# Kernel tuning notes

Measured on AMD Instinct MI355X. Metric: run time of the kernel, lower is better.

The kernel has to match this reference:

```python
import jax, jax.numpy as jnp
import numpy as np

B, D, H, T = 8192, 256, 266, 20  # batch, dim, dim+10, num timesteps
LAMBDA = 1.0
SIGMA = 1.0
EPS = 1e-5  # torch BatchNorm1d default eps


def _bn(h, g, b):
    # training-mode BatchNorm1d: biased batch statistics over axis 0
    m = h.mean(0)
    v = h.var(0)
    return g * (h - m) * jax.lax.rsqrt(v + EPS) + b


def _hidden(x, W, b, g, be):
    return jax.nn.relu(_bn(x @ W.T + b, g, be))


def setup_inputs() -> dict:
    key = jax.random.key(0)
    ks = jax.random.split(key, 16)

    def n(k, shape, s=0.05):
        return jax.random.normal(k, shape, jnp.float32) * s

    inp = {}
    inp["x"] = jax.random.normal(ks[0], (B, D), jnp.float32)
    inp["xi"] = jax.random.normal(ks[1], (T, B, D), jnp.float32)
    inp["timegrid"] = jnp.linspace(0.0, 1.0, T + 1).astype(jnp.float32)
    # per-timestep stacks of Linear+BN params (i_h1, h1_h2, h2_o)
    inp["W1"] = n(ks[2], (T, H, D)); inp["b1"] = jnp.zeros((T, H), jnp.float32)
    inp["g1"] = jnp.ones((T, H), jnp.float32); inp["be1"] = jnp.zeros((T, H), jnp.float32)
    inp["W2"] = n(ks[3], (T, H, H)); inp["b2"] = jnp.zeros((T, H), jnp.float32)
    inp["g2"] = jnp.ones((T, H), jnp.float32); inp["be2"] = jnp.zeros((T, H), jnp.float32)
    inp["W3"] = n(ks[4], (T, D, H)); inp["b3"] = jnp.zeros((T, D), jnp.float32)
    # v0 network: hiddenLayer(D,H) -> hiddenLayer(H,H) -> hiddenLayer(H,1)
    inp["vW1"] = n(ks[5], (H, D)); inp["vb1"] = jnp.zeros((H,), jnp.float32)
    inp["vg1"] = jnp.ones((H,), jnp.float32); inp["vbe1"] = jnp.zeros((H,), jnp.float32)
    inp["vW2"] = n(ks[6], (H, H)); inp["vb2"] = jnp.zeros((H,), jnp.float32)
    inp["vg2"] = jnp.ones((H,), jnp.float32); inp["vbe2"] = jnp.zeros((H,), jnp.float32)
    inp["vW3"] = n(ks[7], (1, H)); inp["vb3"] = jnp.zeros((1,), jnp.float32)
    inp["vg3"] = jnp.ones((1,), jnp.float32); inp["vbe3"] = jnp.zeros((1,), jnp.float32)
    return inp


def reference(x, xi, timegrid, W1, b1, g1, be1, W2, b2, g2, be2, W3, b3,
              vW1, vb1, vg1, vbe1, vW2, vb2, vg2, vbe2, vW3, vb3, vg3, vbe3):
    # v0 sub-network evaluated on the initial x (i == 0 branch)
    v0 = _hidden(x, vW1, vb1, vg1, vbe1)
    v0 = _hidden(v0, vW2, vb2, vg2, vbe2)
    v0 = _hidden(v0, vW3, vb3, vg3, vbe3)  # [B, 1]

    hsteps = timegrid[1:] - timegrid[:-1]  # [T]

    def step(carry, inp_t):
        xt, vt = carry
        (W1t, b1t, g1t, be1t, W2t, b2t, g2t, be2t, W3t, b3t, ht, xit) = inp_t
        h1 = _hidden(xt, W1t, b1t, g1t, be1t)
        h2 = _hidden(h1, W2t, b2t, g2t, be2t)
        grad = h2 @ W3t.T + b3t                     # [B, D]
        alpha = -jnp.sqrt(LAMBDA) * grad
        f = jnp.sum(alpha * alpha, axis=1)          # ||alpha||_2^2 per row
        noise = SIGMA * jnp.sqrt(ht) * xit          # sigma*sqrt(h)*xi
        # diag(grad @ noise.T) == row-wise dot product (same math, O(B*D))
        dot = jnp.sum(grad * noise, axis=1)
        vt = vt - (f * ht)[:, None] + dot[:, None]
        xt = xt + alpha * ht + noise
        return (xt, vt), None

    (xT, vT), _ = jax.lax.scan(
        step, (x, v0),
        (W1, b1, g1, be1, W2, b2, g2, be2, W3, b3, hsteps, xi))
    return vT, xT
```

## Files before the change

kernel.cpp:

```cpp
#include <hip/hip_runtime.h>
#include <hip/hip_bf16.h>
#include <math.h>

#define BATCH 8192
#define DDIM 256
#define HDIM 266
#define NPAD 320
#define TSTEPS 20
#define BN_EPS 1e-5f
#define LSTR 72

typedef __attribute__((ext_vector_type(8))) short short8;
typedef __attribute__((ext_vector_type(4))) float f32x4;

__device__ __forceinline__ short f2bf(float f) {
    __hip_bfloat16 h = __float2bfloat16(f);
    return *reinterpret_cast<short*>(&h);
}
__device__ __forceinline__ float bf2f(short s) {
    union { unsigned u; float f; } v;
    v.u = ((unsigned)(unsigned short)s) << 16;
    return v.f;
}

#define SZ_W1B (20L * 320 * 256)
#define SZ_W2B (20L * 320 * 320)
#define SZ_W3B (20L * 256 * 320)
#define SZ_VW1 (320L * 256)
#define SZ_VW2 (320L * 320)
#define SZ_B1P (20L * 320)
#define SZ_B2P (20L * 320)
#define PREP_TOTAL (SZ_W1B + SZ_W2B + SZ_W3B + SZ_VW1 + SZ_VW2 + SZ_B1P + SZ_B2P + 3 * 320)

__global__ __launch_bounds__(256)
void prep_k(short* __restrict__ W1b, const float* __restrict__ W1,
            short* __restrict__ W2b, const float* __restrict__ W2,
            short* __restrict__ W3b, const float* __restrict__ W3,
            short* __restrict__ vW1b, const float* __restrict__ vW1,
            short* __restrict__ vW2b, const float* __restrict__ vW2,
            float* __restrict__ b1p, const float* __restrict__ b1,
            float* __restrict__ b2p, const float* __restrict__ b2,
            float* __restrict__ vb1p, const float* __restrict__ vb1,
            float* __restrict__ vb2p, const float* __restrict__ vb2,
            float* __restrict__ vW3p, const float* __restrict__ vW3)
{
    long idx = (long)blockIdx.x * 256 + threadIdx.x;
    if (idx < SZ_W1B) {
        long k = idx % 256, r = (idx / 256) % 320, t = idx / (256L * 320);
        float v = (r < HDIM) ? W1[((size_t)t * HDIM + r) * 256 + k] : 0.0f;
        W1b[idx] = f2bf(v); return;
    }
    idx -= SZ_W1B;
    if (idx < SZ_W2B) {
        long k = idx % 320, r = (idx / 320) % 320, t = idx / (320L * 320);
        float v = (r < HDIM && k < HDIM) ? W2[((size_t)t * HDIM + r) * HDIM + k] : 0.0f;
        W2b[idx] = f2bf(v); return;
    }
    idx -= SZ_W2B;
    if (idx < SZ_W3B) {
        long k = idx % 320, r = (idx / 320) % 256, t = idx / (320L * 256);
        float v = (k < HDIM) ? W3[((size_t)t * 256 + r) * HDIM + k] : 0.0f;
        W3b[idx] = f2bf(v); return;
    }
    idx -= SZ_W3B;
    if (idx < SZ_VW1) {
        long k = idx % 256, r = idx / 256;
        float v = (r < HDIM) ? vW1[(size_t)r * 256 + k] : 0.0f;
        vW1b[idx] = f2bf(v); return;
    }
    idx -= SZ_VW1;
    if (idx < SZ_VW2) {
        long k = idx % 320, r = idx / 320;
        float v = (r < HDIM && k < HDIM) ? vW2[(size_t)r * HDIM + k] : 0.0f;
        vW2b[idx] = f2bf(v); return;
    }
    idx -= SZ_VW2;
    if (idx < SZ_B1P) { long n = idx % 320, t = idx / 320;
        b1p[idx] = (n < HDIM) ? b1[(size_t)t * HDIM + n] : 0.0f; return; }
    idx -= SZ_B1P;
    if (idx < SZ_B2P) { long n = idx % 320, t = idx / 320;
        b2p[idx] = (n < HDIM) ? b2[(size_t)t * HDIM + n] : 0.0f; return; }
    idx -= SZ_B2P;
    if (idx < 320) { vb1p[idx] = (idx < HDIM) ? vb1[idx] : 0.0f; return; }
    idx -= 320;
    if (idx < 320) { vb2p[idx] = (idx < HDIM) ? vb2[idx] : 0.0f; return; }
    idx -= 320;
    if (idx < 320) { vW3p[idx] = (idx < HDIM) ? vW3[idx] : 0.0f; return; }
}

__global__ __launch_bounds__(256)
void init_k(const float* __restrict__ x, short* __restrict__ xtb,
            float* __restrict__ zbase, int zcount)
{
    int i = blockIdx.x * 256 + threadIdx.x;
    if (i < BATCH * DDIM) xtb[i] = f2bf(x[i]);
    if (i < zcount) zbase[i] = 0.0f;
}

__global__ __launch_bounds__(256)
void gemm1_k(const short* __restrict__ A, const short* __restrict__ W,
             const float* __restrict__ biasp, short* __restrict__ C,
             float* __restrict__ csum, float* __restrict__ csq)
{
    __shared__ __align__(16) short As[64 * LSTR];
    __shared__ __align__(16) short Bs[64 * LSTR];
    const int tid = threadIdx.x;
    const int col0 = blockIdx.x * 64, row0 = blockIdx.y * 64;
    const int lane = tid & 63, w = tid >> 6, q = lane >> 4, m = lane & 15;
    const int wr = (w >> 1) * 32, wc = (w & 1) * 32;
    const int srow = tid >> 2, kq = (tid & 3) * 8;

    const short* ap = A + (size_t)(row0 + srow) * DDIM + kq;
    const short* wp = W + (size_t)(col0 + srow) * DDIM + kq;
    short8 ra0 = *(const short8*)ap;
    short8 ra1 = *(const short8*)(ap + 32);
    short8 rw0 = *(const short8*)wp;
    short8 rw1 = *(const short8*)(wp + 32);

    f32x4 acc[2][2];
    #pragma unroll
    for (int i = 0; i < 2; ++i)
        #pragma unroll
        for (int j = 0; j < 2; ++j) acc[i][j] = (f32x4){0.f, 0.f, 0.f, 0.f};

    #pragma unroll
    for (int kt = 0; kt < 4; ++kt) {
        *(short8*)&As[srow * LSTR + kq]      = ra0;
        *(short8*)&As[srow * LSTR + kq + 32] = ra1;
        *(short8*)&Bs[srow * LSTR + kq]      = rw0;
        *(short8*)&Bs[srow * LSTR + kq + 32] = rw1;
        __syncthreads();
        if (kt < 3) {
            ap += 64; wp += 64;
            ra0 = *(const short8*)ap; ra1 = *(const short8*)(ap + 32);
            rw0 = *(const short8*)wp; rw1 = *(const short8*)(wp + 32);
        }
        #pragma unroll
        for (int kk = 0; kk < 2; ++kk) {
            short8 fa0 = *(const short8*)&As[(wr + m)      * LSTR + kk * 32 + q * 8];
            short8 fa1 = *(const short8*)&As[(wr + 16 + m) * LSTR + kk * 32 + q * 8];
            short8 fb0 = *(const short8*)&Bs[(wc + m)      * LSTR + kk * 32 + q * 8];
            short8 fb1 = *(const short8*)&Bs[(wc + 16 + m) * LSTR + kk * 32 + q * 8];
            acc[0][0] = __builtin_amdgcn_mfma_f32_16x16x32_bf16(fa0, fb0, acc[0][0], 0, 0, 0);
            acc[0][1] = __builtin_amdgcn_mfma_f32_16x16x32_bf16(fa0, fb1, acc[0][1], 0, 0, 0);
            acc[1][0] = __builtin_amdgcn_mfma_f32_16x16x32_bf16(fa1, fb0, acc[1][0], 0, 0, 0);
            acc[1][1] = __builtin_amdgcn_mfma_f32_16x16x32_bf16(fa1, fb1, acc[1][1], 0, 0, 0);
        }
        __syncthreads();
    }

    float cs[2], cq[2];
    #pragma unroll
    for (int j = 0; j < 2; ++j) {
        const int col = col0 + wc + j * 16 + m;
        const float bv = biasp[col];
        float s = 0.0f, sq = 0.0f;
        #pragma unroll
        for (int i = 0; i < 2; ++i)
            #pragma unroll
            for (int r = 0; r < 4; ++r) {
                float v = acc[i][j][r] + bv;
                int row = row0 + wr + i * 16 + q * 4 + r;
                C[(size_t)row * NPAD + col] = f2bf(v);
                s += v; sq += v * v;
            }
        cs[j] = s; cq[j] = sq;
    }
    #pragma unroll
    for (int j = 0; j < 2; ++j) {
        cs[j] += __shfl_xor(cs[j], 16); cs[j] += __shfl_xor(cs[j], 32);
        cq[j] += __shfl_xor(cq[j], 16); cq[j] += __shfl_xor(cq[j], 32);
    }
    float* reds = (float*)As;
    float* redq = (float*)Bs;
    if (q == 0) {
        #pragma unroll
        for (int j = 0; j < 2; ++j) {
            reds[(w >> 1) * 64 + wc + j * 16 + m] = cs[j];
            redq[(w >> 1) * 64 + wc + j * 16 + m] = cq[j];
        }
    }
    __syncthreads();
    if (tid < 64) {
        int col = col0 + tid;
        if (col < HDIM) {
            atomicAdd(&csum[col], reds[tid] + reds[64 + tid]);
            atomicAdd(&csq[col],  redq[tid] + redq[64 + tid]);
        }
    }
}

__global__ __launch_bounds__(256)
void gemm2_k(const short* __restrict__ A, const short* __restrict__ W,
             const float* __restrict__ biasp,
             const float* __restrict__ csum_in, const float* __restrict__ csq_in,
             const float* __restrict__ g, const float* __restrict__ be,
             short* __restrict__ C,
             float* __restrict__ csum_out, float* __restrict__ csq_out)
{
    __shared__ __align__(16) short As[32 * LSTR];
    __shared__ __align__(16) short Bs[160 * LSTR];
    __shared__ float sS[NPAD], sT[NPAD];
    const int tid = threadIdx.x;
    for (int k = tid; k < NPAD; k += 256) {
        float s = 0.0f, t = 0.0f;
        if (k < HDIM) {
            float mn = csum_in[k] * (1.0f / BATCH);
            float vr = csq_in[k] * (1.0f / BATCH) - mn * mn;
            float rs = rsqrtf(fmaxf(vr, 0.0f) + BN_EPS);
            s = g[k] * rs;
            t = be[k] - mn * s;
        }
        sS[k] = s; sT[k] = t;
    }
    __syncthreads();

    const int col0 = blockIdx.x * 160, row0 = blockIdx.y * 32;
    const int lane = tid & 63, w = tid >> 6, q = lane >> 4, m = lane & 15;
    const int rh = w >> 1, ch = w & 1;
    const int srowA = tid >> 3, kqA = (tid & 7) * 8;

    const short* ap = A + (size_t)(row0 + srowA) * NPAD + kqA;
    short8 rA = *(const short8*)ap;
    short8 rB[5];
    #pragma unroll
    for (int i = 0; i < 5; ++i) {
        int s = tid + 256 * i;
        rB[i] = *(const short8*)(W + (size_t)(col0 + (s >> 3)) * NPAD + ((s & 7) * 8));
    }

    f32x4 acc[5];
    #pragma unroll
    for (int j = 0; j < 5; ++j) acc[j] = (f32x4){0.f, 0.f, 0.f, 0.f};

    #pragma unroll
    for (int kt = 0; kt < 5; ++kt) {
        short8 ta;
        const int kb = kt * 64 + kqA;
        #pragma unroll
        for (int j = 0; j < 8; ++j) {
            float f = bf2f(rA[j]);
            f = fmaxf(f * sS[kb + j] + sT[kb + j], 0.0f);
            ta[j] = f2bf(f);
        }
        *(short8*)&As[srowA * LSTR + kqA] = ta;
        #pragma unroll
        for (int i = 0; i < 5; ++i) {
            int s = tid + 256 * i;
            *(short8*)&Bs[(s >> 3) * LSTR + (s & 7) * 8] = rB[i];
        }
        __syncthreads();
        if (kt < 4) {
            ap += 64;
            rA = *(const short8*)ap;
            #pragma unroll
            for (int i = 0; i < 5; ++i) {
                int s = tid + 256 * i;
                rB[i] = *(const short8*)(W + (size_t)(col0 + (s >> 3)) * NPAD
                                         + (kt + 1) * 64 + ((s & 7) * 8));
            }
        }
        #pragma unroll
        for (int kk = 0; kk < 2; ++kk) {
            short8 fa = *(const short8*)&As[(rh * 16 + m) * LSTR + kk * 32 + q * 8];
            #pragma unroll
            for (int j = 0; j < 5; ++j) {
                short8 fb = *(const short8*)&Bs[(ch * 80 + j * 16 + m) * LSTR + kk * 32 + q * 8];
                acc[j] = __builtin_amdgcn_mfma_f32_16x16x32_bf16(fa, fb, acc[j], 0, 0, 0);
            }
        }
        __syncthreads();
    }

    float csv[5], cqv[5];
    #pragma unroll
    for (int j = 0; j < 5; ++j) {
        const int col = col0 + ch * 80 + j * 16 + m;
        const float bv = biasp[col];
        float s = 0.0f, sq = 0.0f;
        #pragma unroll
        for (int r = 0; r < 4; ++r) {
            float v = acc[j][r] + bv;
            int row = row0 + rh * 16 + q * 4 + r;
            C[(size_t)row * NPAD + col] = f2bf(v);
            s += v; sq += v * v;
        }
        csv[j] = s; cqv[j] = sq;
    }
    #pragma unroll
    for (int j = 0; j < 5; ++j) {
        csv[j] += __shfl_xor(csv[j], 16); csv[j] += __shfl_xor(csv[j], 32);
        cqv[j] += __shfl_xor(cqv[j], 16); cqv[j] += __shfl_xor(cqv[j], 32);
    }
    float* redS = (float*)As;
    float* redQ = redS + 320;
    if (q == 0) {
        #pragma unroll
        for (int j = 0; j < 5; ++j) {
            redS[rh * 160 + ch * 80 + j * 16 + m] = csv[j];
            redQ[rh * 160 + ch * 80 + j * 16 + m] = cqv[j];
        }
    }
    __syncthreads();
    if (tid < 160) {
        int col = col0 + tid;
        if (col < HDIM) {
            atomicAdd(&csum_out[col], redS[tid] + redS[160 + tid]);
            atomicAdd(&csq_out[col],  redQ[tid] + redQ[160 + tid]);
        }
    }
}

__global__ __launch_bounds__(256)
void gemm3_k(const short* __restrict__ A, const short* __restrict__ W,
             const float* __restrict__ bias,
             const float* __restrict__ csum_in, const float* __restrict__ csq_in,
             const float* __restrict__ g, const float* __restrict__ be,
             const float* __restrict__ xi_t,
             short* __restrict__ xtb, float* __restrict__ xout,
             float* __restrict__ ftab, float* __restrict__ dtab,
             const float* __restrict__ tg, int t, int last)
{
    __shared__ __align__(16) short As[32 * LSTR];
    __shared__ __align__(16) short Bs[128 * LSTR];
    __shared__ float sS[NPAD], sT[NPAD];
    const int tid = threadIdx.x;
    for (int k = tid; k < NPAD; k += 256) {
        float s = 0.0f, tt = 0.0f;
        if (k < HDIM) {
            float mn = csum_in[k] * (1.0f / BATCH);
            float vr = csq_in[k] * (1.0f / BATCH) - mn * mn;
            float rs = rsqrtf(fmaxf(vr, 0.0f) + BN_EPS);
            s = g[k] * rs;
            tt = be[k] - mn * s;
        }
        sS[k] = s; sT[k] = tt;
    }
    __syncthreads();

    const int col0 = blockIdx.x * 128, row0 = blockIdx.y * 32;
    const int lane = tid & 63, w = tid >> 6, q = lane >> 4, m = lane & 15;
    const int rh = w >> 1, ch = w & 1;
    const int srowA = tid >> 3, kqA = (tid & 7) * 8;

    const short* ap = A + (size_t)(row0 + srowA) * NPAD + kqA;
    short8 rA = *(const short8*)ap;
    short8 rB[4];
    #pragma unroll
    for (int i = 0; i < 4; ++i) {
        int s = tid + 256 * i;
        rB[i] = *(const short8*)(W + (size_t)(col0 + (s >> 3)) * NPAD + ((s & 7) * 8));
    }

    f32x4 acc[4];
    #pragma unroll
    for (int j = 0; j < 4; ++j) acc[j] = (f32x4){0.f, 0.f, 0.f, 0.f};

    #pragma unroll
    for (int kt = 0; kt < 5; ++kt) {
        short8 ta;
        const int kb = kt * 64 + kqA;
        #pragma unroll
        for (int j = 0; j < 8; ++j) {
            float f = bf2f(rA[j]);
            f = fmaxf(f * sS[kb + j] + sT[kb + j], 0.0f);
            ta[j] = f2bf(f);
        }
        *(short8*)&As[srowA * LSTR + kqA] = ta;
        #pragma unroll
        for (int i = 0; i < 4; ++i) {
            int s = tid + 256 * i;
            *(short8*)&Bs[(s >> 3) * LSTR + (s & 7) * 8] = rB[i];
        }
        __syncthreads();
        if (kt < 4) {
            ap += 64;
            rA = *(const short8*)ap;
            #pragma unroll
            for (int i = 0; i < 4; ++i) {
                int s = tid + 256 * i;
                rB[i] = *(const short8*)(W + (size_t)(col0 + (s >> 3)) * NPAD
                                         + (kt + 1) * 64 + ((s & 7) * 8));
            }
        }
        #pragma unroll
        for (int kk = 0; kk < 2; ++kk) {
            short8 fa = *(const short8*)&As[(rh * 16 + m) * LSTR + kk * 32 + q * 8];
            #pragma unroll
            for (int j = 0; j < 4; ++j) {
                short8 fb = *(const short8*)&Bs[(ch * 64 + j * 16 + m) * LSTR + kk * 32 + q * 8];
                acc[j] = __builtin_amdgcn_mfma_f32_16x16x32_bf16(fa, fb, acc[j], 0, 0, 0);
            }
        }
        __syncthreads();
    }

    const float ht = tg[t + 1] - tg[t];
    const float sn = sqrtf(ht);
    float fr[4] = {0.f, 0.f, 0.f, 0.f};
    float dr[4] = {0.f, 0.f, 0.f, 0.f};
    #pragma unroll
    for (int j = 0; j < 4; ++j) {
        const int col = col0 + ch * 64 + j * 16 + m;
        const float bv = bias[col];
        #pragma unroll
        for (int r = 0; r < 4; ++r) {
            const int row = row0 + rh * 16 + q * 4 + r;
            size_t idx = (size_t)row * DDIM + col;
            float grad = acc[j][r] + bv;
            float noise = sn * xi_t[idx];
            float nx = bf2f(xtb[idx]) - grad * ht + noise;
            xtb[idx] = f2bf(nx);
            if (last) xout[idx] = nx;
            fr[r] += grad * grad;
            dr[r] += grad * noise;
        }
    }
    #pragma unroll
    for (int r = 0; r < 4; ++r) {
        fr[r] += __shfl_xor(fr[r], 1); dr[r] += __shfl_xor(dr[r], 1);
        fr[r] += __shfl_xor(fr[r], 2); dr[r] += __shfl_xor(dr[r], 2);
        fr[r] += __shfl_xor(fr[r], 4); dr[r] += __shfl_xor(dr[r], 4);
        fr[r] += __shfl_xor(fr[r], 8); dr[r] += __shfl_xor(dr[r], 8);
    }
    if (m == 0) {
        #pragma unroll
        for (int r = 0; r < 4; ++r) {
            const int row = row0 + rh * 16 + q * 4 + r;
            atomicAdd(&ftab[row], fr[r]);
            atomicAdd(&dtab[row], dr[r]);
        }
    }
}

__global__ __launch_bounds__(256)
void vrow_k(const short* __restrict__ A,
            const float* __restrict__ csum_in, const float* __restrict__ csq_in,
            const float* __restrict__ g, const float* __restrict__ be,
            const float* __restrict__ vW3p, const float* __restrict__ vb3,
            float* __restrict__ pre3, float* __restrict__ s3, float* __restrict__ q3)
{
    __shared__ float sS[NPAD], sT[NPAD];
    __shared__ float wred[8];
    const int tid = threadIdx.x;
    for (int k = tid; k < NPAD; k += 256) {
        float s = 0.0f, t = 0.0f;
        if (k < HDIM) {
            float mn = csum_in[k] * (1.0f / BATCH);
            float vr = csq_in[k] * (1.0f / BATCH) - mn * mn;
            float rs = rsqrtf(fmaxf(vr, 0.0f) + BN_EPS);
            s = g[k] * rs;
            t = be[k] - mn * s;
        }
        sS[k] = s; sT[k] = t;
    }
    __syncthreads();
    const int wave = tid >> 6, lane = tid & 63;
    const int row = blockIdx.x * 4 + wave;
    float sum = 0.0f;
    #pragma unroll
    for (int c = 0; c < 5; ++c) {
        int k = c * 64 + lane;
        float v = fmaxf(bf2f(A[(size_t)row * NPAD + k]) * sS[k] + sT[k], 0.0f);
        sum += v * vW3p[k];
    }
    sum += __shfl_xor(sum, 1);  sum += __shfl_xor(sum, 2);
    sum += __shfl_xor(sum, 4);  sum += __shfl_xor(sum, 8);
    sum += __shfl_xor(sum, 16); sum += __shfl_xor(sum, 32);
    if (lane == 0) {
        float p = sum + vb3[0];
        pre3[row] = p;
        wred[wave] = p;
        wred[4 + wave] = p * p;
    }
    __syncthreads();
    if (tid == 0) {
        atomicAdd(s3, wred[0] + wred[1] + wred[2] + wred[3]);
        atomicAdd(q3, wred[4] + wred[5] + wred[6] + wred[7]);
    }
}

__global__ __launch_bounds__(256)
void v3b_k(const float* __restrict__ pre3,
           const float* __restrict__ s3, const float* __restrict__ q3,
           const float* __restrict__ vg3, const float* __restrict__ vbe3,
           float* __restrict__ vt)
{
    int i = blockIdx.x * 256 + threadIdx.x;
    float mn = s3[0] * (1.0f / BATCH);
    float va = fmaxf(q3[0] * (1.0f / BATCH) - mn * mn, 0.0f);
    float rs = rsqrtf(va + BN_EPS);
    if (i < BATCH) vt[i] = fmaxf(vg3[0] * (pre3[i] - mn) * rs + vbe3[0], 0.0f);
}

__global__ __launch_bounds__(256)
void final_v_k(const float* __restrict__ vt,
               const float* __restrict__ ftab, const float* __restrict__ dtab,
               const float* __restrict__ tg, float* __restrict__ outv)
{
    int i = blockIdx.x * 256 + threadIdx.x;
    if (i >= BATCH) return;
    float v = vt[i];
    for (int t = 0; t < TSTEPS; ++t) {
        float ht = tg[t + 1] - tg[t];
        v += dtab[(size_t)t * BATCH + i] - ftab[(size_t)t * BATCH + i] * ht;
    }
    outv[i] = v;
}

extern "C" void kernel_launch(void* const* d_in, const int* in_sizes, int n_in,
                              void* d_out, int out_size, void* d_ws, size_t ws_size,
                              hipStream_t stream)
{
    const float* x    = (const float*)d_in[0];
    const float* xi   = (const float*)d_in[1];
    const float* tg   = (const float*)d_in[2];
    const float* W1   = (const float*)d_in[3];
    const float* b1   = (const float*)d_in[4];
    const float* g1   = (const float*)d_in[5];
    const float* be1  = (const float*)d_in[6];
    const float* W2   = (const float*)d_in[7];
    const float* b2   = (const float*)d_in[8];
    const float* g2   = (const float*)d_in[9];
    const float* be2  = (const float*)d_in[10];
    const float* W3   = (const float*)d_in[11];
    const float* b3   = (const float*)d_in[12];
    const float* vW1  = (const float*)d_in[13];
    const float* vb1  = (const float*)d_in[14];
    const float* vg1  = (const float*)d_in[15];
    const float* vbe1 = (const float*)d_in[16];
    const float* vW2  = (const float*)d_in[17];
    const float* vb2  = (const float*)d_in[18];
    const float* vg2  = (const float*)d_in[19];
    const float* vbe2 = (const float*)d_in[20];
    const float* vW3  = (const float*)d_in[21];
    const float* vb3  = (const float*)d_in[22];
    const float* vg3  = (const float*)d_in[23];
    const float* vbe3 = (const float*)d_in[24];

    float* out  = (float*)d_out;
    float* xout = out + BATCH;

    short* xtb  = (short*)d_ws;
    short* hp1  = xtb + (size_t)BATCH * DDIM;
    short* hp2  = hp1 + (size_t)BATCH * NPAD;
    short* W1b  = hp2 + (size_t)BATCH * NPAD;
    short* W2b  = W1b + SZ_W1B;
    short* W3b  = W2b + SZ_W2B;
    short* vW1b = W3b + SZ_W3B;
    short* vW2b = vW1b + SZ_VW1;
    float* fbase = (float*)(vW2b + SZ_VW2);
    float* b1p  = fbase;
    float* b2p  = b1p + TSTEPS * NPAD;
    float* vb1p = b2p + TSTEPS * NPAD;
    float* vb2p = vb1p + NPAD;
    float* vW3p = vb2p + NPAD;
    float* vt   = vW3p + NPAD;
    float* pre3 = vt + BATCH;
    float* ftab = pre3 + BATCH;
    float* dtab = ftab + (size_t)TSTEPS * BATCH;
    float* csA  = dtab + (size_t)TSTEPS * BATCH;
    float* cqA  = csA + 21 * NPAD;
    float* csB  = cqA + 21 * NPAD;
    float* cqB  = csB + 21 * NPAD;
    float* s3   = cqB + 21 * NPAD;
    float* q3   = s3 + 1;
    const int zcount = 2 * TSTEPS * BATCH + 4 * 21 * NPAD + 2;

    dim3 blk(256);
    dim3 g1g(5, BATCH / 64);
    dim3 g2g(2, BATCH / 32);
    dim3 g3g(2, BATCH / 32);

    init_k<<<dim3((BATCH * DDIM + 255) / 256), blk, 0, stream>>>(x, xtb, ftab, zcount);
    prep_k<<<dim3((int)((PREP_TOTAL + 255) / 256)), blk, 0, stream>>>(
        W1b, W1, W2b, W2, W3b, W3, vW1b, vW1, vW2b, vW2,
        b1p, b1, b2p, b2, vb1p, vb1, vb2p, vb2, vW3p, vW3);

    float* csV1 = csA + 20 * NPAD; float* cqV1 = cqA + 20 * NPAD;
    float* csV2 = csB + 20 * NPAD; float* cqV2 = cqB + 20 * NPAD;
    gemm1_k<<<g1g, blk, 0, stream>>>(xtb, vW1b, vb1p, hp1, csV1, cqV1);
    gemm2_k<<<g2g, blk, 0, stream>>>(hp1, vW2b, vb2p, csV1, cqV1, vg1, vbe1,
                                     hp2, csV2, cqV2);
    vrow_k<<<dim3(BATCH / 4), blk, 0, stream>>>(hp2, csV2, cqV2, vg2, vbe2,
                                                vW3p, vb3, pre3, s3, q3);
    v3b_k<<<dim3(BATCH / 256), blk, 0, stream>>>(pre3, s3, q3, vg3, vbe3, vt);

    for (int t = 0; t < TSTEPS; ++t) {
        gemm1_k<<<g1g, blk, 0, stream>>>(
            xtb, W1b + (size_t)t * NPAD * DDIM, b1p + t * NPAD,
            hp1, csA + t * NPAD, cqA + t * NPAD);
        gemm2_k<<<g2g, blk, 0, stream>>>(
            hp1, W2b + (size_t)t * NPAD * NPAD, b2p + t * NPAD,
            csA + t * NPAD, cqA + t * NPAD, g1 + t * HDIM, be1 + t * HDIM,
            hp2, csB + t * NPAD, cqB + t * NPAD);
        gemm3_k<<<g3g, blk, 0, stream>>>(
            hp2, W3b + (size_t)t * DDIM * NPAD, b3 + t * DDIM,
            csB + t * NPAD, cqB + t * NPAD, g2 + t * HDIM, be2 + t * HDIM,
            xi + (size_t)t * BATCH * DDIM, xtb, xout,
            ftab + (size_t)t * BATCH, dtab + (size_t)t * BATCH,
            tg, t, (t == TSTEPS - 1) ? 1 : 0);
    }
    final_v_k<<<dim3(BATCH / 256), blk, 0, stream>>>(vt, ftab, dtab, tg, out);
}
```

Baseline: 1.144 ms.

## Fuse all timesteps into one cooperative persistent kernel with on-chip activations

```diff
diff --git a/kernel.cpp b/kernel.cpp
--- a/kernel.cpp
+++ b/kernel.cpp
@@ -1,6 +1,9 @@
 #include <hip/hip_runtime.h>
+#include <hip/hip_cooperative_groups.h>
 #include <hip/hip_bf16.h>
 #include <math.h>
+
+namespace cg = cooperative_groups;
 
 #define BATCH 8192
 #define DDIM 256
@@ -30,7 +33,8 @@
 #define SZ_VW2 (320L * 320)
 #define SZ_B1P (20L * 320)
 #define SZ_B2P (20L * 320)
-#define PREP_TOTAL (SZ_W1B + SZ_W2B + SZ_W3B + SZ_VW1 + SZ_VW2 + SZ_B1P + SZ_B2P + 3 * 320)
+#define ZCOUNT (4L * 21 * NPAD + 2)
+#define PREP_TOTAL (SZ_W1B + SZ_W2B + SZ_W3B + SZ_VW1 + SZ_VW2 + SZ_B1P + SZ_B2P + 3 * 320 + ZCOUNT)
 
 __global__ __launch_bounds__(256)
 void prep_k(short* __restrict__ W1b, const float* __restrict__ W1,
@@ -42,7 +46,8 @@
             float* __restrict__ b2p, const float* __restrict__ b2,
             float* __restrict__ vb1p, const float* __restrict__ vb1,
             float* __restrict__ vb2p, const float* __restrict__ vb2,
-            float* __restrict__ vW3p, const float* __restrict__ vW3)
+            float* __restrict__ vW3p, const float* __restrict__ vW3,
+            float* __restrict__ zbase)
 {
     long idx = (long)blockIdx.x * 256 + threadIdx.x;
     if (idx < SZ_W1B) {
@@ -86,203 +91,113 @@
     if (idx < 320) { vb2p[idx] = (idx < HDIM) ? vb2[idx] : 0.0f; return; }
     idx -= 320;
     if (idx < 320) { vW3p[idx] = (idx < HDIM) ? vW3[idx] : 0.0f; return; }
-}
-
-__global__ __launch_bounds__(256)
-void init_k(const float* __restrict__ x, short* __restrict__ xtb,
-            float* __restrict__ zbase, int zcount)
-{
-    int i = blockIdx.x * 256 + threadIdx.x;
-    if (i < BATCH * DDIM) xtb[i] = f2bf(x[i]);
-    if (i < zcount) zbase[i] = 0.0f;
-}
-
-__global__ __launch_bounds__(256)
-void gemm1_k(const short* __restrict__ A, const short* __restrict__ W,
-             const float* __restrict__ biasp, short* __restrict__ C,
-             float* __restrict__ csum, float* __restrict__ csq)
-{
-    __shared__ __align__(16) short As[64 * LSTR];
-    __shared__ __align__(16) short Bs[64 * LSTR];
-    const int tid = threadIdx.x;
-    const int col0 = blockIdx.x * 64, row0 = blockIdx.y * 64;
-    const int lane = tid & 63, w = tid >> 6, q = lane >> 4, m = lane & 15;
-    const int wr = (w >> 1) * 32, wc = (w & 1) * 32;
-    const int srow = tid >> 2, kq = (tid & 3) * 8;
-
-    const short* ap = A + (size_t)(row0 + srow) * DDIM + kq;
-    const short* wp = W + (size_t)(col0 + srow) * DDIM + kq;
-    short8 ra0 = *(const short8*)ap;
-    short8 ra1 = *(const short8*)(ap + 32);
-    short8 rw0 = *(const short8*)wp;
-    short8 rw1 = *(const short8*)(wp + 32);
-
-    f32x4 acc[2][2];
-    #pragma unroll
-    for (int i = 0; i < 2; ++i)
-        #pragma unroll
-        for (int j = 0; j < 2; ++j) acc[i][j] = (f32x4){0.f, 0.f, 0.f, 0.f};
-
-    #pragma unroll
-    for (int kt = 0; kt < 4; ++kt) {
-        *(short8*)&As[srow * LSTR + kq]      = ra0;
-        *(short8*)&As[srow * LSTR + kq + 32] = ra1;
-        *(short8*)&Bs[srow * LSTR + kq]      = rw0;
-        *(short8*)&Bs[srow * LSTR + kq + 32] = rw1;
-        __syncthreads();
-        if (kt < 3) {
-            ap += 64; wp += 64;
-            ra0 = *(const short8*)ap; ra1 = *(const short8*)(ap + 32);
-            rw0 = *(const short8*)wp; rw1 = *(const short8*)(wp + 32);
-        }
-        #pragma unroll
-        for (int kk = 0; kk < 2; ++kk) {
-            short8 fa0 = *(const short8*)&As[(wr + m)      * LSTR + kk * 32 + q * 8];
-            short8 fa1 = *(const short8*)&As[(wr + 16 + m) * LSTR + kk * 32 + q * 8];
-            short8 fb0 = *(const short8*)&Bs[(wc + m)      * LSTR + kk * 32 + q * 8];
-            short8 fb1 = *(const short8*)&Bs[(wc + 16 + m) * LSTR + kk * 32 + q * 8];
-            acc[0][0] = __builtin_amdgcn_mfma_f32_16x16x32_bf16(fa0, fb0, acc[0][0], 0, 0, 0);
-            acc[0][1] = __builtin_amdgcn_mfma_f32_16x16x32_bf16(fa0, fb1, acc[0][1], 0, 0, 0);
-            acc[1][0] = __builtin_amdgcn_mfma_f32_16x16x32_bf16(fa1, fb0, acc[1][0], 0, 0, 0);
-            acc[1][1] = __builtin_amdgcn_mfma_f32_16x16x32_bf16(fa1, fb1, acc[1][1], 0, 0, 0);
-        }
-        __syncthreads();
-    }
-
-    float cs[2], cq[2];
-    #pragma unroll
-    for (int j = 0; j < 2; ++j) {
-        const int col = col0 + wc + j * 16 + m;
-        const float bv = biasp[col];
-        float s = 0.0f, sq = 0.0f;
-        #pragma unroll
-        for (int i = 0; i < 2; ++i)
-            #pragma unroll
-            for (int r = 0; r < 4; ++r) {
-                float v = acc[i][j][r] + bv;
-                int row = row0 + wr + i * 16 + q * 4 + r;
-                C[(size_t)row * NPAD + col] = f2bf(v);
-                s += v; sq += v * v;
-            }
-        cs[j] = s; cq[j] = sq;
-    }
-    #pragma unroll
-    for (int j = 0; j < 2; ++j) {
-        cs[j] += __shfl_xor(cs[j], 16); cs[j] += __shfl_xor(cs[j], 32);
-        cq[j] += __shfl_xor(cq[j], 16); cq[j] += __shfl_xor(cq[j], 32);
-    }
-    float* reds = (float*)As;
-    float* redq = (float*)Bs;
-    if (q == 0) {
-        #pragma unroll
-        for (int j = 0; j < 2; ++j) {
-            reds[(w >> 1) * 64 + wc + j * 16 + m] = cs[j];
-            redq[(w >> 1) * 64 + wc + j * 16 + m] = cq[j];
-        }
-    }
-    __syncthreads();
-    if (tid < 64) {
-        int col = col0 + tid;
-        if (col < HDIM) {
-            atomicAdd(&csum[col], reds[tid] + reds[64 + tid]);
-            atomicAdd(&csq[col],  redq[tid] + redq[64 + tid]);
-        }
-    }
-}
-
-__global__ __launch_bounds__(256)
-void gemm2_k(const short* __restrict__ A, const short* __restrict__ W,
-             const float* __restrict__ biasp,
-             const float* __restrict__ csum_in, const float* __restrict__ csq_in,
-             const float* __restrict__ g, const float* __restrict__ be,
-             short* __restrict__ C,
-             float* __restrict__ csum_out, float* __restrict__ csq_out)
-{
-    __shared__ __align__(16) short As[32 * LSTR];
-    __shared__ __align__(16) short Bs[160 * LSTR];
-    __shared__ float sS[NPAD], sT[NPAD];
-    const int tid = threadIdx.x;
-    for (int k = tid; k < NPAD; k += 256) {
+    idx -= 320;
+    if (idx < ZCOUNT) { zbase[idx] = 0.0f; return; }
+}
+
+__device__ __forceinline__ void bn_coeff(const float* __restrict__ cs,
+                                         const float* __restrict__ cq,
+                                         const float* __restrict__ g,
+                                         const float* __restrict__ be,
+                                         float* sS, float* sT, int tid)
+{
+    for (int k = tid; k < NPAD; k += 512) {
         float s = 0.0f, t = 0.0f;
         if (k < HDIM) {
-            float mn = csum_in[k] * (1.0f / BATCH);
-            float vr = csq_in[k] * (1.0f / BATCH) - mn * mn;
+            float mn = cs[k] * (1.0f / BATCH);
+            float vr = cq[k] * (1.0f / BATCH) - mn * mn;
             float rs = rsqrtf(fmaxf(vr, 0.0f) + BN_EPS);
             s = g[k] * rs;
             t = be[k] - mn * s;
         }
         sS[k] = s; sT[k] = t;
     }
-    __syncthreads();
-
-    const int col0 = blockIdx.x * 160, row0 = blockIdx.y * 32;
-    const int lane = tid & 63, w = tid >> 6, q = lane >> 4, m = lane & 15;
-    const int rh = w >> 1, ch = w & 1;
+}
+
+template<int NJ>
+__device__ __forceinline__ void preload_w(const short* __restrict__ Wt, int KLEN,
+                                          short8* rW, int tid)
+{
+    #pragma unroll
+    for (int i = 0; i < NJ; ++i) {
+        int s = tid + 512 * i;
+        rW[i] = *(const short8*)(Wt + (size_t)(s >> 3) * KLEN + ((s & 7) * 8));
+    }
+}
+
+template<int NKT, int NJ, bool BN>
+__device__ __forceinline__ void gemm_phase(
+    const short* __restrict__ Wt, const short* Asrc, short* As1, short* Bs,
+    const float* sS, const float* sT, f32x4* acc, short8* rW, int tid)
+{
+    const int lane = tid & 63, q = lane >> 4, m = lane & 15;
+    const int w = tid >> 6, rh = w >> 2, ch = w & 3;
     const int srowA = tid >> 3, kqA = (tid & 7) * 8;
-
-    const short* ap = A + (size_t)(row0 + srowA) * NPAD + kqA;
-    short8 rA = *(const short8*)ap;
-    short8 rB[5];
-    #pragma unroll
-    for (int i = 0; i < 5; ++i) {
-        int s = tid + 256 * i;
-        rB[i] = *(const short8*)(W + (size_t)(col0 + (s >> 3)) * NPAD + ((s & 7) * 8));
-    }
-
-    f32x4 acc[5];
-    #pragma unroll
-    for (int j = 0; j < 5; ++j) acc[j] = (f32x4){0.f, 0.f, 0.f, 0.f};
-
-    #pragma unroll
-    for (int kt = 0; kt < 5; ++kt) {
-        short8 ta;
-        const int kb = kt * 64 + kqA;
-        #pragma unroll
-        for (int j = 0; j < 8; ++j) {
-            float f = bf2f(rA[j]);
-            f = fmaxf(f * sS[kb + j] + sT[kb + j], 0.0f);
-            ta[j] = f2bf(f);
-        }
-        *(short8*)&As[srowA * LSTR + kqA] = ta;
-        #pragma unroll
-        for (int i = 0; i < 5; ++i) {
-            int s = tid + 256 * i;
-            *(short8*)&Bs[(s >> 3) * LSTR + (s & 7) * 8] = rB[i];
-        }
-        __syncthreads();
-        if (kt < 4) {
-            ap += 64;
-            rA = *(const short8*)ap;
-            #pragma unroll
-            for (int i = 0; i < 5; ++i) {
-                int s = tid + 256 * i;
-                rB[i] = *(const short8*)(W + (size_t)(col0 + (s >> 3)) * NPAD
+    const int KLEN = NKT * 64;
+
+    #pragma unroll
+    for (int kt = 0; kt < NKT; ++kt) {
+        if (BN) {
+            if (tid < 256) {
+                short8 v = *(const short8*)&Asrc[(kt * 32 + srowA) * LSTR + kqA];
+                short8 ta;
+                #pragma unroll
+                for (int j = 0; j < 8; ++j) {
+                    int k = kt * 64 + kqA + j;
+                    float f = bf2f(v[j]);
+                    f = fmaxf(f * sS[k] + sT[k], 0.0f);
+                    ta[j] = f2bf(f);
+                }
+                *(short8*)&As1[srowA * LSTR + kqA] = ta;
+            }
+        }
+        #pragma unroll
+        for (int i = 0; i < NJ; ++i) {
+            int s = tid + 512 * i;
+            *(short8*)&Bs[(s >> 3) * LSTR + (s & 7) * 8] = rW[i];
+        }
+        __syncthreads();
+        if (kt < NKT - 1) {
+            #pragma unroll
+            for (int i = 0; i < NJ; ++i) {
+                int s = tid + 512 * i;
+                rW[i] = *(const short8*)(Wt + (size_t)(s >> 3) * KLEN
                                          + (kt + 1) * 64 + ((s & 7) * 8));
             }
         }
+        const short* ab = BN ? As1 : (Asrc + kt * 32 * LSTR);
         #pragma unroll
         for (int kk = 0; kk < 2; ++kk) {
-            short8 fa = *(const short8*)&As[(rh * 16 + m) * LSTR + kk * 32 + q * 8];
-            #pragma unroll
-            for (int j = 0; j < 5; ++j) {
-                short8 fb = *(const short8*)&Bs[(ch * 80 + j * 16 + m) * LSTR + kk * 32 + q * 8];
+            short8 fa = *(const short8*)&ab[(rh * 16 + m) * LSTR + kk * 32 + q * 8];
+            #pragma unroll
+            for (int j = 0; j < NJ; ++j) {
+                short8 fb = *(const short8*)&Bs[(ch * (NJ * 16) + j * 16 + m) * LSTR
+                                                + kk * 32 + q * 8];
                 acc[j] = __builtin_amdgcn_mfma_f32_16x16x32_bf16(fa, fb, acc[j], 0, 0, 0);
             }
         }
         __syncthreads();
     }
-
+}
+
+__device__ __forceinline__ void epi_store_stats(
+    const f32x4* acc, const float* __restrict__ bias, short* dst,
+    float* redS, float* redQ, float* __restrict__ csum, float* __restrict__ csq,
+    int tid)
+{
+    const int lane = tid & 63, q = lane >> 4, m = lane & 15;
+    const int w = tid >> 6, rh = w >> 2, ch = w & 3;
     float csv[5], cqv[5];
     #pragma unroll
     for (int j = 0; j < 5; ++j) {
-        const int col = col0 + ch * 80 + j * 16 + m;
-        const float bv = biasp[col];
+        const int col = ch * 80 + j * 16 + m;
+        const float bv = bias[col];
         float s = 0.0f, sq = 0.0f;
         #pragma unroll
         for (int r = 0; r < 4; ++r) {
             float v = acc[j][r] + bv;
-            int row = row0 + rh * 16 + q * 4 + r;
-            C[(size_t)row * NPAD + col] = f2bf(v);
+            int row = rh * 16 + q * 4 + r;
+            dst[((col >> 6) * 32 + row) * LSTR + (col & 63)] = f2bf(v);
             s += v; sq += v * v;
         }
         csv[j] = s; cqv[j] = sq;
@@ -292,220 +207,202 @@
         csv[j] += __shfl_xor(csv[j], 16); csv[j] += __shfl_xor(csv[j], 32);
         cqv[j] += __shfl_xor(cqv[j], 16); cqv[j] += __shfl_xor(cqv[j], 32);
     }
-    float* redS = (float*)As;
-    float* redQ = redS + 320;
     if (q == 0) {
         #pragma unroll
         for (int j = 0; j < 5; ++j) {
-            redS[rh * 160 + ch * 80 + j * 16 + m] = csv[j];
-            redQ[rh * 160 + ch * 80 + j * 16 + m] = cqv[j];
+            int col = ch * 80 + j * 16 + m;
+            redS[rh * NPAD + col] = csv[j];
+            redQ[rh * NPAD + col] = cqv[j];
         }
     }
     __syncthreads();
-    if (tid < 160) {
-        int col = col0 + tid;
-        if (col < HDIM) {
-            atomicAdd(&csum_out[col], redS[tid] + redS[160 + tid]);
-            atomicAdd(&csq_out[col],  redQ[tid] + redQ[160 + tid]);
-        }
-    }
-}
-
-__global__ __launch_bounds__(256)
-void gemm3_k(const short* __restrict__ A, const short* __restrict__ W,
-             const float* __restrict__ bias,
-             const float* __restrict__ csum_in, const float* __restrict__ csq_in,
-             const float* __restrict__ g, const float* __restrict__ be,
-             const float* __restrict__ xi_t,
-             short* __restrict__ xtb, float* __restrict__ xout,
-             float* __restrict__ ftab, float* __restrict__ dtab,
-             const float* __restrict__ tg, int t, int last)
-{
-    __shared__ __align__(16) short As[32 * LSTR];
-    __shared__ __align__(16) short Bs[128 * LSTR];
+    if (tid < HDIM) {
+        atomicAdd(&csum[tid], redS[tid] + redS[NPAD + tid]);
+        atomicAdd(&csq[tid],  redQ[tid] + redQ[NPAD + tid]);
+    }
+}
+
+struct PArgs {
+    const float* x; const float* xi; const float* tg;
+    const short* W1b; const short* W2b; const short* W3b;
+    const short* vW1b; const short* vW2b;
+    const float* b1p; const float* b2p; const float* b3;
+    const float* vb1p; const float* vb2p; const float* vW3p; const float* vb3;
+    const float* g1; const float* be1; const float* g2; const float* be2;
+    const float* vg1; const float* vbe1; const float* vg2; const float* vbe2;
+    const float* vg3; const float* vbe3;
+    float* csA; float* cqA; float* csB; float* cqB;
+    float* s3; float* q3;
+    float* out; float* xout;
+};
+
+__global__ __launch_bounds__(512)
+void persist_k(PArgs p)
+{
+    cg::grid_group grid = cg::this_grid();
+
+    __shared__ __align__(16) short xbuf[128 * LSTR];
+    __shared__ __align__(16) short h1buf[160 * LSTR];
+    __shared__ __align__(16) short h2buf[160 * LSTR];
+    __shared__ __align__(16) short Bs[320 * LSTR];
+    __shared__ __align__(16) short As1[32 * LSTR];
     __shared__ float sS[NPAD], sT[NPAD];
+    __shared__ float redS[2 * NPAD], redQ[2 * NPAD];
+    __shared__ float redF[128], redD[128];
+    __shared__ float pre3L[32], vacc[32];
+
     const int tid = threadIdx.x;
-    for (int k = tid; k < NPAD; k += 256) {
-        float s = 0.0f, tt = 0.0f;
-        if (k < HDIM) {
-            float mn = csum_in[k] * (1.0f / BATCH);
-            float vr = csq_in[k] * (1.0f / BATCH) - mn * mn;
-            float rs = rsqrtf(fmaxf(vr, 0.0f) + BN_EPS);
-            s = g[k] * rs;
-            tt = be[k] - mn * s;
-        }
-        sS[k] = s; sT[k] = tt;
-    }
+    const int row0 = blockIdx.x * 32;
+    const int lane = tid & 63, w = tid >> 6, q = lane >> 4, m = lane & 15;
+    const int rh = w >> 2, ch = w & 3;
+
+    for (int i2 = tid; i2 < 32 * 256; i2 += 512) {
+        int row = i2 >> 8, col = i2 & 255;
+        xbuf[((col >> 6) * 32 + row) * LSTR + (col & 63)] =
+            f2bf(p.x[(size_t)(row0 + row) * DDIM + col]);
+    }
+    if (tid < 32) vacc[tid] = 0.0f;
+
+    short8 rW[5];
+    f32x4 acc[5];
+
+    preload_w<5>(p.vW1b, DDIM, rW, tid);
+    #pragma unroll
+    for (int j = 0; j < 5; ++j) acc[j] = (f32x4){0.f, 0.f, 0.f, 0.f};
     __syncthreads();
-
-    const int col0 = blockIdx.x * 128, row0 = blockIdx.y * 32;
-    const int lane = tid & 63, w = tid >> 6, q = lane >> 4, m = lane & 15;
-    const int rh = w >> 1, ch = w & 1;
-    const int srowA = tid >> 3, kqA = (tid & 7) * 8;
-
-    const short* ap = A + (size_t)(row0 + srowA) * NPAD + kqA;
-    short8 rA = *(const short8*)ap;
-    short8 rB[4];
-    #pragma unroll
-    for (int i = 0; i < 4; ++i) {
-        int s = tid + 256 * i;
-        rB[i] = *(const short8*)(W + (size_t)(col0 + (s >> 3)) * NPAD + ((s & 7) * 8));
-    }
-
-    f32x4 acc[4];
-    #pragma unroll
-    for (int j = 0; j < 4; ++j) acc[j] = (f32x4){0.f, 0.f, 0.f, 0.f};
-
-    #pragma unroll
-    for (int kt = 0; kt < 5; ++kt) {
-        short8 ta;
-        const int kb = kt * 64 + kqA;
-        #pragma unroll
-        for (int j = 0; j < 8; ++j) {
-            float f = bf2f(rA[j]);
-            f = fmaxf(f * sS[kb + j] + sT[kb + j], 0.0f);
-            ta[j] = f2bf(f);
-        }
-        *(short8*)&As[srowA * LSTR + kqA] = ta;
-        #pragma unroll
-        for (int i = 0; i < 4; ++i) {
-            int s = tid + 256 * i;
-            *(short8*)&Bs[(s >> 3) * LSTR + (s & 7) * 8] = rB[i];
-        }
-        __syncthreads();
-        if (kt < 4) {
-            ap += 64;
-            rA = *(const short8*)ap;
-            #pragma unroll
-            for (int i = 0; i < 4; ++i) {
-                int s = tid + 256 * i;
-                rB[i] = *(const short8*)(W + (size_t)(col0 + (s >> 3)) * NPAD
-                                         + (kt + 1) * 64 + ((s & 7) * 8));
-            }
-        }
-        #pragma unroll
-        for (int kk = 0; kk < 2; ++kk) {
-            short8 fa = *(const short8*)&As[(rh * 16 + m) * LSTR + kk * 32 + q * 8];
-            #pragma unroll
-            for (int j = 0; j < 4; ++j) {
-                short8 fb = *(const short8*)&Bs[(ch * 64 + j * 16 + m) * LSTR + kk * 32 + q * 8];
-                acc[j] = __builtin_amdgcn_mfma_f32_16x16x32_bf16(fa, fb, acc[j], 0, 0, 0);
-            }
-        }
-        __syncthreads();
-    }
-
-    const float ht = tg[t + 1] - tg[t];
-    const float sn = sqrtf(ht);
-    float fr[4] = {0.f, 0.f, 0.f, 0.f};
-    float dr[4] = {0.f, 0.f, 0.f, 0.f};
-    #pragma unroll
-    for (int j = 0; j < 4; ++j) {
-        const int col = col0 + ch * 64 + j * 16 + m;
-        const float bv = bias[col];
+    gemm_phase<4, 5, false>(p.vW1b, xbuf, As1, Bs, sS, sT, acc, rW, tid);
+    epi_store_stats(acc, p.vb1p, h1buf, redS, redQ,
+                    p.csA + 20 * NPAD, p.cqA + 20 * NPAD, tid);
+    preload_w<5>(p.vW2b, NPAD, rW, tid);
+    grid.sync();
+
+    bn_coeff(p.csA + 20 * NPAD, p.cqA + 20 * NPAD, p.vg1, p.vbe1, sS, sT, tid);
+    #pragma unroll
+    for (int j = 0; j < 5; ++j) acc[j] = (f32x4){0.f, 0.f, 0.f, 0.f};
+    __syncthreads();
+    gemm_phase<5, 5, true>(p.vW2b, h1buf, As1, Bs, sS, sT, acc, rW, tid);
+    epi_store_stats(acc, p.vb2p, h2buf, redS, redQ,
+                    p.csB + 20 * NPAD, p.cqB + 20 * NPAD, tid);
+    grid.sync();
+
+    bn_coeff(p.csB + 20 * NPAD, p.cqB + 20 * NPAD, p.vg2, p.vbe2, sS, sT, tid);
+    __syncthreads();
+    {
+        const int wv = tid >> 6, ln = tid & 63;
+        float ps = 0.0f, pq = 0.0f;
+        #pragma unroll
+        for (int r4 = 0; r4 < 4; ++r4) {
+            int row = wv * 4 + r4;
+            float sum = 0.0f;
+            #pragma unroll
+            for (int c = 0; c < 5; ++c) {
+                int k = c * 64 + ln;
+                float v = fmaxf(bf2f(h2buf[(c * 32 + row) * LSTR + ln]) * sS[k] + sT[k], 0.0f);
+                sum += v * p.vW3p[k];
+            }
+            sum += __shfl_xor(sum, 1);  sum += __shfl_xor(sum, 2);
+            sum += __shfl_xor(sum, 4);  sum += __shfl_xor(sum, 8);
+            sum += __shfl_xor(sum, 16); sum += __shfl_xor(sum, 32);
+            if (ln == 0) {
+                float pv = sum + p.vb3[0];
+                pre3L[row] = pv;
+                ps += pv; pq += pv * pv;
+            }
+        }
+        if (ln == 0) { redF[wv] = ps; redD[wv] = pq; }
+        __syncthreads();
+        if (tid == 0) {
+            float a = 0.0f, b = 0.0f;
+            #pragma unroll
+            for (int i = 0; i < 8; ++i) { a += redF[i]; b += redD[i]; }
+            atomicAdd(p.s3, a); atomicAdd(p.q3, b);
+        }
+    }
+
+    for (int t = 0; t < TSTEPS; ++t) {
+        preload_w<5>(p.W1b + (size_t)t * NPAD * DDIM, DDIM, rW, tid);
+        #pragma unroll
+        for (int j = 0; j < 5; ++j) acc[j] = (f32x4){0.f, 0.f, 0.f, 0.f};
+        gemm_phase<4, 5, false>(p.W1b + (size_t)t * NPAD * DDIM, xbuf, As1, Bs,
+                                sS, sT, acc, rW, tid);
+        epi_store_stats(acc, p.b1p + t * NPAD, h1buf, redS, redQ,
+                        p.csA + t * NPAD, p.cqA + t * NPAD, tid);
+        preload_w<5>(p.W2b + (size_t)t * NPAD * NPAD, NPAD, rW, tid);
+        grid.sync();
+
+        bn_coeff(p.csA + t * NPAD, p.cqA + t * NPAD,
+                 p.g1 + (size_t)t * HDIM, p.be1 + (size_t)t * HDIM, sS, sT, tid);
+        #pragma unroll
+        for (int j = 0; j < 5; ++j) acc[j] = (f32x4){0.f, 0.f, 0.f, 0.f};
+        __syncthreads();
+        gemm_phase<5, 5, true>(p.W2b + (size_t)t * NPAD * NPAD, h1buf, As1, Bs,
+                               sS, sT, acc, rW, tid);
+        epi_store_stats(acc, p.b2p + t * NPAD, h2buf, redS, redQ,
+                        p.csB + t * NPAD, p.cqB + t * NPAD, tid);
+        preload_w<4>(p.W3b + (size_t)t * DDIM * NPAD, NPAD, rW, tid);
+        grid.sync();
+
+        bn_coeff(p.csB + t * NPAD, p.cqB + t * NPAD,
+                 p.g2 + (size_t)t * HDIM, p.be2 + (size_t)t * HDIM, sS, sT, tid);
+        #pragma unroll
+        for (int j = 0; j < 4; ++j) acc[j] = (f32x4){0.f, 0.f, 0.f, 0.f};
+        __syncthreads();
+        gemm_phase<5, 4, true>(p.W3b + (size_t)t * DDIM * NPAD, h2buf, As1, Bs,
+                               sS, sT, acc, rW, tid);
+
+        const float ht = p.tg[t + 1] - p.tg[t];
+        const float sn = sqrtf(ht);
+        const float* xi_t = p.xi + (size_t)t * BATCH * DDIM;
+        float fr[4] = {0.f, 0.f, 0.f, 0.f};
+        float dr[4] = {0.f, 0.f, 0.f, 0.f};
+        #pragma unroll
+        for (int j = 0; j < 4; ++j) {
+            const int col = ch * 64 + j * 16 + m;
+            const float bv = p.b3[(size_t)t * DDIM + col];
+            #pragma unroll
+            for (int r = 0; r < 4; ++r) {
+                const int lr = rh * 16 + q * 4 + r;
+                const size_t idx = (size_t)(row0 + lr) * DDIM + col;
+                float grad = acc[j][r] + bv;
+                float noise = sn * xi_t[idx];
+                const int xo = (ch * 32 + lr) * LSTR + (j * 16 + m);
+                float nx = bf2f(xbuf[xo]) - grad * ht + noise;
+                xbuf[xo] = f2bf(nx);
+                if (t == TSTEPS - 1) p.xout[idx] = nx;
+                fr[r] += grad * grad;
+                dr[r] += grad * noise;
+            }
+        }
         #pragma unroll
         for (int r = 0; r < 4; ++r) {
-            const int row = row0 + rh * 16 + q * 4 + r;
-            size_t idx = (size_t)row * DDIM + col;
-            float grad = acc[j][r] + bv;
-            float noise = sn * xi_t[idx];
-            float nx = bf2f(xtb[idx]) - grad * ht + noise;
-            xtb[idx] = f2bf(nx);
-            if (last) xout[idx] = nx;
-            fr[r] += grad * grad;
-            dr[r] += grad * noise;
-        }
-    }
-    #pragma unroll
-    for (int r = 0; r < 4; ++r) {
-        fr[r] += __shfl_xor(fr[r], 1); dr[r] += __shfl_xor(dr[r], 1);
-        fr[r] += __shfl_xor(fr[r], 2); dr[r] += __shfl_xor(dr[r], 2);
-        fr[r] += __shfl_xor(fr[r], 4); dr[r] += __shfl_xor(dr[r], 4);
-        fr[r] += __shfl_xor(fr[r], 8); dr[r] += __shfl_xor(dr[r], 8);
-    }
-    if (m == 0) {
-        #pragma unroll
-        for (int r = 0; r < 4; ++r) {
-            const int row = row0 + rh * 16 + q * 4 + r;
-            atomicAdd(&ftab[row], fr[r]);
-            atomicAdd(&dtab[row], dr[r]);
-        }
-    }
-}
-
-__global__ __launch_bounds__(256)
-void vrow_k(const short* __restrict__ A,
-            const float* __restrict__ csum_in, const float* __restrict__ csq_in,
-            const float* __restrict__ g, const float* __restrict__ be,
-            const float* __restrict__ vW3p, const float* __restrict__ vb3,
-            float* __restrict__ pre3, float* __restrict__ s3, float* __restrict__ q3)
-{
-    __shared__ float sS[NPAD], sT[NPAD];
-    __shared__ float wred[8];
-    const int tid = threadIdx.x;
-    for (int k = tid; k < NPAD; k += 256) {
-        float s = 0.0f, t = 0.0f;
-        if (k < HDIM) {
-            float mn = csum_in[k] * (1.0f / BATCH);
-            float vr = csq_in[k] * (1.0f / BATCH) - mn * mn;
-            float rs = rsqrtf(fmaxf(vr, 0.0f) + BN_EPS);
-            s = g[k] * rs;
-            t = be[k] - mn * s;
-        }
-        sS[k] = s; sT[k] = t;
-    }
-    __syncthreads();
-    const int wave = tid >> 6, lane = tid & 63;
-    const int row = blockIdx.x * 4 + wave;
-    float sum = 0.0f;
-    #pragma unroll
-    for (int c = 0; c < 5; ++c) {
-        int k = c * 64 + lane;
-        float v = fmaxf(bf2f(A[(size_t)row * NPAD + k]) * sS[k] + sT[k], 0.0f);
-        sum += v * vW3p[k];
-    }
-    sum += __shfl_xor(sum, 1);  sum += __shfl_xor(sum, 2);
-    sum += __shfl_xor(sum, 4);  sum += __shfl_xor(sum, 8);
-    sum += __shfl_xor(sum, 16); sum += __shfl_xor(sum, 32);
-    if (lane == 0) {
-        float p = sum + vb3[0];
-        pre3[row] = p;
-        wred[wave] = p;
-        wred[4 + wave] = p * p;
-    }
-    __syncthreads();
-    if (tid == 0) {
-        atomicAdd(s3, wred[0] + wred[1] + wred[2] + wred[3]);
-        atomicAdd(q3, wred[4] + wred[5] + wred[6] + wred[7]);
-    }
-}
-
-__global__ __launch_bounds__(256)
-void v3b_k(const float* __restrict__ pre3,
-           const float* __restrict__ s3, const float* __restrict__ q3,
-           const float* __restrict__ vg3, const float* __restrict__ vbe3,
-           float* __restrict__ vt)
-{
-    int i = blockIdx.x * 256 + threadIdx.x;
-    float mn = s3[0] * (1.0f / BATCH);
-    float va = fmaxf(q3[0] * (1.0f / BATCH) - mn * mn, 0.0f);
-    float rs = rsqrtf(va + BN_EPS);
-    if (i < BATCH) vt[i] = fmaxf(vg3[0] * (pre3[i] - mn) * rs + vbe3[0], 0.0f);
-}
-
-__global__ __launch_bounds__(256)
-void final_v_k(const float* __restrict__ vt,
-               const float* __restrict__ ftab, const float* __restrict__ dtab,
-               const float* __restrict__ tg, float* __restrict__ outv)
-{
-    int i = blockIdx.x * 256 + threadIdx.x;
-    if (i >= BATCH) return;
-    float v = vt[i];
-    for (int t = 0; t < TSTEPS; ++t) {
-        float ht = tg[t + 1] - tg[t];
-        v += dtab[(size_t)t * BATCH + i] - ftab[(size_t)t * BATCH + i] * ht;
-    }
-    outv[i] = v;
+            fr[r] += __shfl_xor(fr[r], 1); dr[r] += __shfl_xor(dr[r], 1);
+            fr[r] += __shfl_xor(fr[r], 2); dr[r] += __shfl_xor(dr[r], 2);
+            fr[r] += __shfl_xor(fr[r], 4); dr[r] += __shfl_xor(dr[r], 4);
+            fr[r] += __shfl_xor(fr[r], 8); dr[r] += __shfl_xor(dr[r], 8);
+        }
+        if (m == 0) {
+            #pragma unroll
+            for (int r = 0; r < 4; ++r) {
+                redF[ch * 32 + rh * 16 + q * 4 + r] = fr[r];
+                redD[ch * 32 + rh * 16 + q * 4 + r] = dr[r];
+            }
+        }
+        __syncthreads();
+        if (tid < 32) {
+            float fsum = redF[tid] + redF[32 + tid] + redF[64 + tid] + redF[96 + tid];
+            float dsum = redD[tid] + redD[32 + tid] + redD[64 + tid] + redD[96 + tid];
+            vacc[tid] += dsum - fsum * ht;
+        }
+        __syncthreads();
+    }
+
+    if (tid < 32) {
+        float mn = p.s3[0] * (1.0f / BATCH);
+        float va = fmaxf(p.q3[0] * (1.0f / BATCH) - mn * mn, 0.0f);
+        float rs = rsqrtf(va + BN_EPS);
+        float v0 = fmaxf(p.vg3[0] * (pre3L[tid] - mn) * rs + p.vbe3[0], 0.0f);
+        p.out[row0 + tid] = v0 + vacc[tid];
+    }
 }
 
 extern "C" void kernel_launch(void* const* d_in, const int* in_sizes, int n_in,
@@ -541,65 +438,41 @@
     float* out  = (float*)d_out;
     float* xout = out + BATCH;
 
-    short* xtb  = (short*)d_ws;
-    short* hp1  = xtb + (size_t)BATCH * DDIM;
-    short* hp2  = hp1 + (size_t)BATCH * NPAD;
-    short* W1b  = hp2 + (size_t)BATCH * NPAD;
+    short* W1b  = (short*)d_ws;
     short* W2b  = W1b + SZ_W1B;
     short* W3b  = W2b + SZ_W2B;
     short* vW1b = W3b + SZ_W3B;
     short* vW2b = vW1b + SZ_VW1;
-    float* fbase = (float*)(vW2b + SZ_VW2);
-    float* b1p  = fbase;
+    float* b1p  = (float*)(vW2b + SZ_VW2);
     float* b2p  = b1p + TSTEPS * NPAD;
     float* vb1p = b2p + TSTEPS * NPAD;
     float* vb2p = vb1p + NPAD;
     float* vW3p = vb2p + NPAD;
-    float* vt   = vW3p + NPAD;
-    float* pre3 = vt + BATCH;
-    float* ftab = pre3 + BATCH;
-    float* dtab = ftab + (size_t)TSTEPS * BATCH;
-    float* csA  = dtab + (size_t)TSTEPS * BATCH;
+    float* csA  = vW3p + NPAD;
     float* cqA  = csA + 21 * NPAD;
     float* csB  = cqA + 21 * NPAD;
     float* cqB  = csB + 21 * NPAD;
     float* s3   = cqB + 21 * NPAD;
     float* q3   = s3 + 1;
-    const int zcount = 2 * TSTEPS * BATCH + 4 * 21 * NPAD + 2;
-
-    dim3 blk(256);
-    dim3 g1g(5, BATCH / 64);
-    dim3 g2g(2, BATCH / 32);
-    dim3 g3g(2, BATCH / 32);
-
-    init_k<<<dim3((BATCH * DDIM + 255) / 256), blk, 0, stream>>>(x, xtb, ftab, zcount);
-    prep_k<<<dim3((int)((PREP_TOTAL + 255) / 256)), blk, 0, stream>>>(
+
+    prep_k<<<dim3((int)((PREP_TOTAL + 255) / 256)), dim3(256), 0, stream>>>(
         W1b, W1, W2b, W2, W3b, W3, vW1b, vW1, vW2b, vW2,
-        b1p, b1, b2p, b2, vb1p, vb1, vb2p, vb2, vW3p, vW3);
-
-    float* csV1 = csA + 20 * NPAD; float* cqV1 = cqA + 20 * NPAD;
-    float* csV2 = csB + 20 * NPAD; float* cqV2 = cqB + 20 * NPAD;
-    gemm1_k<<<g1g, blk, 0, stream>>>(xtb, vW1b, vb1p, hp1, csV1, cqV1);
-    gemm2_k<<<g2g, blk, 0, stream>>>(hp1, vW2b, vb2p, csV1, cqV1, vg1, vbe1,
-                                     hp2, csV2, cqV2);
-    vrow_k<<<dim3(BATCH / 4), blk, 0, stream>>>(hp2, csV2, cqV2, vg2, vbe2,
-                                                vW3p, vb3, pre3, s3, q3);
-    v3b_k<<<dim3(BATCH / 256), blk, 0, stream>>>(pre3, s3, q3, vg3, vbe3, vt);
-
-    for (int t = 0; t < TSTEPS; ++t) {
-        gemm1_k<<<g1g, blk, 0, stream>>>(
-            xtb, W1b + (size_t)t * NPAD * DDIM, b1p + t * NPAD,
-            hp1, csA + t * NPAD, cqA + t * NPAD);
-        gemm2_k<<<g2g, blk, 0, stream>>>(
-            hp1, W2b + (size_t)t * NPAD * NPAD, b2p + t * NPAD,
-            csA + t * NPAD, cqA + t * NPAD, g1 + t * HDIM, be1 + t * HDIM,
-            hp2, csB + t * NPAD, cqB + t * NPAD);
-        gemm3_k<<<g3g, blk, 0, stream>>>(
-            hp2, W3b + (size_t)t * DDIM * NPAD, b3 + t * DDIM,
-            csB + t * NPAD, cqB + t * NPAD, g2 + t * HDIM, be2 + t * HDIM,
-            xi + (size_t)t * BATCH * DDIM, xtb, xout,
-            ftab + (size_t)t * BATCH, dtab + (size_t)t * BATCH,
-            tg, t, (t == TSTEPS - 1) ? 1 : 0);
-    }
-    final_v_k<<<dim3(BATCH / 256), blk, 0, stream>>>(vt, ftab, dtab, tg, out);
-}
+        b1p, b1, b2p, b2, vb1p, vb1, vb2p, vb2, vW3p, vW3, csA);
+
+    PArgs pa;
+    pa.x = x; pa.xi = xi; pa.tg = tg;
+    pa.W1b = W1b; pa.W2b = W2b; pa.W3b = W3b;
+    pa.vW1b = vW1b; pa.vW2b = vW2b;
+    pa.b1p = b1p; pa.b2p = b2p; pa.b3 = b3;
+    pa.vb1p = vb1p; pa.vb2p = vb2p; pa.vW3p = vW3p; pa.vb3 = vb3;
+    pa.g1 = g1; pa.be1 = be1; pa.g2 = g2; pa.be2 = be2;
+    pa.vg1 = vg1; pa.vbe1 = vbe1; pa.vg2 = vg2; pa.vbe2 = vbe2;
+    pa.vg3 = vg3; pa.vbe3 = vbe3;
+    pa.csA = csA; pa.cqA = cqA; pa.csB = csB; pa.cqB = cqB;
+    pa.s3 = s3; pa.q3 = q3;
+    pa.out = out; pa.xout = xout;
+
+    void* kargs[] = { (void*)&pa };
+    hipLaunchCooperativeKernel((const void*)persist_k, dim3(BATCH / 32), dim3(512),
+                               kargs, 0, stream);
+}
```

New measurement: 2.148 ms. +87.7%, slower.
